# Kernel optimization log

Hardware: AMD Instinct MI355X
Metric: run time of the kernel (lower is better)

## Reference

```python
import jax, jax.numpy as jnp
import numpy as np

N = 100000      # nodes
E = 320000      # edges
D = 128         # num_node_in_embeddings
DE = 256        # num_edge_in_embeddings = 2*D
NOBJ = 160
NREL = 27
BN_EPS = 1e-5   # eval-mode BatchNorm with running_mean=0, running_var=1


def setup_inputs() -> dict:
    key = jax.random.key(0)
    ks = jax.random.split(key, 24)
    f32 = jnp.float32
    def rn(k, shape, scale=0.05):
        return jax.random.normal(k, shape, f32) * scale
    return {
        "node_feats": jax.random.normal(ks[0], (N, D), f32),
        "edge_index": jax.random.randint(ks[1], (E, 2), 0, N),
        # GCNConv layers (W: [in,out], bias)
        "gcn1_W": rn(ks[2], (D, D // 2)), "gcn1_b": rn(ks[3], (D // 2,)),
        "gcn2_W": rn(ks[4], (D // 2, D)), "gcn2_b": rn(ks[5], (D,)),
        # edge attention (Linear(DE, D//2))
        "eattn_W": rn(ks[6], (DE, D // 2)), "eattn_b": rn(ks[7], (D // 2,)),
        # node attention (Linear(D, DE//2)) and indicator reduction (Linear(DE, DE//2))
        "nattn_W": rn(ks[8], (D, DE // 2)), "nattn_b": rn(ks[9], (DE // 2,)),
        "nred_W": rn(ks[10], (DE, DE // 2)), "nred_b": rn(ks[11], (DE // 2,)),
        # edge MLPs (1x1 Conv1d == Linear)
        "emlp1_W": rn(ks[12], (DE, DE // 2)), "emlp1_b": rn(ks[13], (DE // 2,)),
        "emlp2_W": rn(ks[14], (DE // 2, DE)), "emlp2_b": rn(ks[15], (DE,)),
        # node classification head
        "nlin1_W": rn(ks[16], (D, D // 2)),
        "nbn_g": jnp.ones((D // 2,), f32) + rn(ks[17], (D // 2,)),
        "nbn_b": rn(ks[18], (D // 2,)),
        "nlin2_W": rn(ks[19], (D // 2, NOBJ)),
        # edge classification head
        "elin1_W": rn(ks[20], (DE, DE // 2)),
        "ebn_g": jnp.ones((DE // 2,), f32) + rn(ks[21], (DE // 2,)),
        "ebn_b": rn(ks[22], (DE // 2,)),
        "elin2_W": rn(ks[23], (DE // 2, NREL)),
    }


def _seg_mean(vals, idx, n):
    # torch_scatter 'mean': sum / clamp(count, 1)
    s = jax.ops.segment_sum(vals, idx, num_segments=n)
    c = jax.ops.segment_sum(jnp.ones((vals.shape[0], 1), vals.dtype), idx, num_segments=n)
    return s / jnp.maximum(c, 1.0)


def _gcn_conv(x, src, dst, W, b, n):
    # PyG GCNConv, add_self_loops=True, symmetric normalization.
    lin = x @ W
    deg = jax.ops.segment_sum(jnp.ones((src.shape[0],), x.dtype), dst, num_segments=n) + 1.0
    dis = jax.lax.rsqrt(deg)                       # deg^{-1/2}, includes self-loop
    norm = dis[src] * dis[dst]                     # per-edge norm
    agg = jax.ops.segment_sum(lin[src] * norm[:, None], dst, num_segments=n)
    return agg + lin * (dis * dis)[:, None] + b    # self-loop term + bias


def _bn_eval(x, g, b):
    # eval-mode BatchNorm1d with running_mean=0, running_var=1
    return x * (g / jnp.sqrt(1.0 + BN_EPS)) + b


def reference(node_feats, edge_index, gcn1_W, gcn1_b, gcn2_W, gcn2_b,
              eattn_W, eattn_b, nattn_W, nattn_b, nred_W, nred_b,
              emlp1_W, emlp1_b, emlp2_W, emlp2_b,
              nlin1_W, nbn_g, nbn_b, nlin2_W,
              elin1_W, ebn_g, ebn_b, elin2_W):
    n = node_feats.shape[0]
    src = edge_index[:, 0]
    dst = edge_index[:, 1]

    # edge feature init: [subject, object - subject]  -> [E, DE]
    subj = node_feats[src]
    edge_feats = jnp.concatenate([subj, node_feats[dst] - subj], axis=1)

    # edge attention -> scatter-mean indicators over rows/cols -> node gate
    edge_ind = edge_feats @ eattn_W + eattn_b            # [E, D/2]
    row = _seg_mean(edge_ind, src, n)                    # [N, D/2]
    col = _seg_mean(edge_ind, dst, n)                    # [N, D/2]
    agg_edge_indicator = jax.nn.sigmoid(row * col)

    # two GCN layers (dropout is identity in eval mode)
    h = jax.nn.relu(_gcn_conv(node_feats, src, dst, gcn1_W, gcn1_b, n)) * agg_edge_indicator
    h = jax.nn.relu(_gcn_conv(h, src, dst, gcn2_W, gcn2_b, n))           # [N, D]

    # node attention -> per-edge gate
    node_ind = jax.nn.relu(h @ nattn_W + nattn_b)                        # [N, DE/2]
    econcat = jnp.concatenate([node_ind[src], node_ind[dst]], axis=1)    # [E, DE]
    agg_node_indicator = jax.nn.sigmoid(econcat @ nred_W + nred_b)       # [E, DE/2]

    # edge MLPs (1x1 convs == linears over edges)
    ef = jax.nn.relu(edge_feats @ emlp1_W + emlp1_b) * agg_node_indicator
    ef = jax.nn.relu(ef @ emlp2_W + emlp2_b)                             # [E, DE]

    # node head: linear -> BN(eval) -> leaky_relu(0.2) -> linear -> softmax over classes
    nx = jax.nn.leaky_relu(_bn_eval(h @ nlin1_W, nbn_g, nbn_b), 0.2)
    node_logits = jax.nn.softmax(nx @ nlin2_W, axis=1)                   # [N, NOBJ]

    # edge head: note original applies softmax on dim=1 of [1,E,NREL] -> over EDGES
    ex = jax.nn.leaky_relu(_bn_eval(ef @ elin1_W, ebn_g, ebn_b), 0.2)
    edge_logits = jax.nn.softmax(ex @ elin2_W, axis=0)                   # [E, NREL]

    return (node_logits, edge_logits)
```

## Files before the change

kernel.cpp:

```cpp
#include <hip/hip_runtime.h>

#define NN 100000
#define EE 320000

typedef unsigned int uint32;
typedef __attribute__((ext_vector_type(8))) short bf16x8;
typedef __attribute__((ext_vector_type(4))) float f32x4;

__device__ __forceinline__ float4 ld4(const float* p){ return *(const float4*)p; }
__device__ __forceinline__ void st4(float* p, const float4 v){ *(float4*)p = v; }
__device__ __forceinline__ float sigm(float x){ return 1.f/(1.f + expf(-x)); }
__device__ __forceinline__ short f2b(float f){
  union { float f; uint32 u; } v; v.f = f;
  uint32 r = (v.u + 0x7FFFu + ((v.u>>16)&1u)) >> 16;
  return (short)r;
}

constexpr int EM_STORE=0, EM_BRELU=1, EM_BNLK=2;

template<int K,int NOUT,int EM>
__global__ __launch_bounds__(256) void gemm_k(
    const float* __restrict__ A,
    const float* __restrict__ W, const float* __restrict__ bias,
    const float* __restrict__ bng,
    float* __restrict__ C, int M)
{
  constexpr int CN = NOUT/16;
  __shared__ float As[16][68];
  __shared__ float Ws[16][NOUT];
  const int t  = threadIdx.x;
  const int tx = t & 15, ty = t >> 4;
  const int row0 = blockIdx.x * 64;

  float acc[4][CN];
  #pragma unroll
  for (int i=0;i<4;i++)
    #pragma unroll
    for (int j=0;j<CN;j++) acc[i][j]=0.f;

  const int r_st  = t >> 2;
  const int kq_st = (t & 3) * 4;

  for (int k0=0;k0<K;k0+=16) {
    {
      float4 v = make_float4(0.f,0.f,0.f,0.f);
      const int gr = row0 + r_st;
      if (gr < M) v = ld4(A + (size_t)gr*K + k0 + kq_st);
      As[kq_st+0][r_st]=v.x; As[kq_st+1][r_st]=v.y;
      As[kq_st+2][r_st]=v.z; As[kq_st+3][r_st]=v.w;
    }
    {
      constexpr int C4 = NOUT/4;
      for (int i=t;i<16*C4;i+=256){ int kk=i/C4, c4=(i%C4)*4;
        st4(&Ws[kk][c4], ld4(W + (size_t)(k0+kk)*NOUT + c4)); }
    }
    __syncthreads();
    #pragma unroll
    for (int kk=0;kk<16;kk++){
      float a0,a1,a2,a3;
      { const float4 av = *(const float4*)&As[kk][ty*4]; a0=av.x;a1=av.y;a2=av.z;a3=av.w; }
      float b[CN];
      if constexpr ((CN & 3) == 0) {
        #pragma unroll
        for (int j4=0;j4<CN;j4+=4){
          const float4 bv = *(const float4*)&Ws[kk][tx*CN+j4];
          b[j4]=bv.x;b[j4+1]=bv.y;b[j4+2]=bv.z;b[j4+3]=bv.w; }
      } else {
        #pragma unroll
        for (int j=0;j<CN;j++) b[j]=Ws[kk][tx*CN+j];
      }
      #pragma unroll
      for (int j=0;j<CN;j++){
        acc[0][j]=fmaf(a0,b[j],acc[0][j]);
        acc[1][j]=fmaf(a1,b[j],acc[1][j]);
        acc[2][j]=fmaf(a2,b[j],acc[2][j]);
        acc[3][j]=fmaf(a3,b[j],acc[3][j]);
      }
    }
    __syncthreads();
  }

  float sc[CN], sh[CN];
  if constexpr (EM==EM_BNLK) {
    const float r_ = rsqrtf(1.f + 1e-5f);
    #pragma unroll
    for (int j=0;j<CN;j++){ int c=tx*CN+j; sc[j]=bng[c]*r_; sh[j]=bias[c]; }
  }
  #pragma unroll
  for (int i=0;i<4;i++){
    const int r  = row0 + ty*4+i;
    if (r >= M) continue;
    #pragma unroll
    for (int j=0;j<CN;j++){
      const int c = tx*CN+j;
      float v = acc[i][j];
      if constexpr (EM==EM_BRELU) v = fmaxf(v + bias[c], 0.f);
      else if constexpr (EM==EM_BNLK){ float x = fmaf(v, sc[j], sh[j]); v = (x>0.f)? x : 0.2f*x; }
      C[(size_t)r*NOUT + c] = v;
    }
  }
}

__global__ void k_hist(const int* __restrict__ eidx, int* cntS, int* cntD, int E){
  int e = blockIdx.x*256+threadIdx.x; if (e>=E) return;
  atomicAdd(&cntS[eidx[2*e]], 1);
  atomicAdd(&cntD[eidx[2*e+1]], 1);
}
__global__ void k_scan_sum(const int* __restrict__ cnt, int* bsum, int n){
  __shared__ int red[256];
  const int b=blockIdx.x, t=threadIdx.x;
  int s=0;
  for (int i=b*1024+t; i<n && i<(b+1)*1024; i+=256) s += cnt[i];
  red[t]=s; __syncthreads();
  for (int o=128;o;o>>=1){ if(t<o) red[t]+=red[t+o]; __syncthreads(); }
  if (t==0) bsum[b]=red[0];
}
__global__ void k_scan_top(int* bsum, int nb){
  __shared__ int sh[256];
  const int t=threadIdx.x;
  int v=(t<nb)?bsum[t]:0;
  sh[t]=v; __syncthreads();
  for (int o=1;o<256;o<<=1){
    int u=0; if(t>=o) u=sh[t-o];
    __syncthreads();
    sh[t]+=u;
    __syncthreads();
  }
  if (t<nb) bsum[t]=sh[t]-v;
}
__global__ void k_scan_out(const int* __restrict__ cnt, const int* __restrict__ bofs,
                           int* __restrict__ off, int n){
  __shared__ int sh[256];
  const int b=blockIdx.x, t=threadIdx.x;
  const int base=b*1024+t*4;
  int c0=0,c1=0,c2=0,c3=0;
  if(base+0<n)c0=cnt[base+0];
  if(base+1<n)c1=cnt[base+1];
  if(base+2<n)c2=cnt[base+2];
  if(base+3<n)c3=cnt[base+3];
  int s=c0+c1+c2+c3;
  sh[t]=s; __syncthreads();
  int v=s;
  for (int o=1;o<256;o<<=1){
    int u=0; if(t>=o) u=sh[t-o];
    __syncthreads();
    sh[t]+=u;
    __syncthreads();
  }
  const int tofs = sh[t]-v + bofs[b];
  if(base+0<n) off[base+0]=tofs;
  if(base+1<n) off[base+1]=tofs+c0;
  if(base+2<n) off[base+2]=tofs+c0+c1;
  if(base+3<n) off[base+3]=tofs+c0+c1+c2;
}
__global__ void k_copyoff(const int* __restrict__ off, int* __restrict__ cur, int n, int E){
  int i=blockIdx.x*256+threadIdx.x;
  if (i<n) cur[i]=off[i];
}
__global__ void k_setend(int* offS, int* offD, int n, int E){
  if (threadIdx.x==0 && blockIdx.x==0){ offS[n]=E; offD[n]=E; }
}
__global__ void k_fill(const int* __restrict__ eidx, int* curS, int* curD,
                       int* __restrict__ csrS, int* __restrict__ csrD, int E){
  int e=blockIdx.x*256+threadIdx.x; if (e>=E) return;
  const int s=eidx[2*e], d=eidx[2*e+1];
  csrS[atomicAdd(&curS[s],1)] = d;
  csrD[atomicAdd(&curD[d],1)] = s;
}
__global__ void k_dis(const int* __restrict__ cntD, float* __restrict__ dis, int n){
  int i=blockIdx.x*256+threadIdx.x; if(i>=n)return;
  dis[i]=rsqrtf((float)cntD[i]+1.f);
}

__global__ void k_wprep(const float* __restrict__ eattnW, const float* __restrict__ gcn1W,
                        float* __restrict__ Wcat){
  int idx=blockIdx.x*256+threadIdx.x; if (idx>=128*192) return;
  int k=idx/192, c=idx-k*192;
  float v;
  if (c<64)       v = eattnW[(size_t)(128+k)*64 + c];
  else if (c<128) v = eattnW[(size_t)k*64 + (c-64)] - eattnW[(size_t)(128+k)*64 + (c-64)];
  else            v = gcn1W[(size_t)k*64 + (c-128)];
  Wcat[idx]=v;
}

template<int NC>
__global__ void k_gather(const float* __restrict__ src, int stride, int colbase,
                         const int* __restrict__ off, const int* __restrict__ csr,
                         float* __restrict__ out, int n){
  constexpr int TPN = NC/4;
  const int t=threadIdx.x;
  const int node = blockIdx.x*(256/TPN) + t/TPN; if (node>=n) return;
  const int cq = (t%TPN)*4;
  const int j1=off[node+1];
  float4 acc = make_float4(0.f,0.f,0.f,0.f);
  for (int j=off[node]; j<j1; ++j){
    const float4 v = ld4(src + (size_t)csr[j]*stride + colbase + cq);
    acc.x+=v.x; acc.y+=v.y; acc.z+=v.z; acc.w+=v.w;
  }
  st4(out + (size_t)node*NC + cq, acc);
}

__global__ void k_aei3(const float* __restrict__ TUL, const float* __restrict__ Q,
                       const float* __restrict__ S, const int* __restrict__ cntS,
                       const int* __restrict__ cntD, const float* __restrict__ bias,
                       float* __restrict__ aei, int n){
  int idx=blockIdx.x*256+threadIdx.x; if (idx>=n*16) return;
  const int i=idx>>4, cq=(idx&15)*4;
  const float cS=(float)cntS[i], cD=(float)cntD[i];
  const float iS=1.f/fmaxf(cS,1.f), iD=1.f/fmaxf(cD,1.f);
  const float* tul = TUL + (size_t)i*192;
  const float4 T4=ld4(tul+cq), U4=ld4(tul+64+cq);
  const float4 Q4=ld4(Q+(size_t)i*64+cq), S4=ld4(S+(size_t)i*64+cq), b4=ld4(bias+cq);
  float4 o;
  o.x=sigm(((cS*(U4.x+b4.x)+Q4.x)*iS) * ((cD*(T4.x+b4.x)+S4.x)*iD));
  o.y=sigm(((cS*(U4.y+b4.y)+Q4.y)*iS) * ((cD*(T4.y+b4.y)+S4.y)*iD));
  o.z=sigm(((cS*(U4.z+b4.z)+Q4.z)*iS) * ((cD*(T4.z+b4.z)+S4.z)*iD));
  o.w=sigm(((cS*(U4.w+b4.w)+Q4.w)*iS) * ((cD*(T4.w+b4.w)+S4.w)*iD));
  st4(aei + (size_t)i*64 + cq, o);
}

template<int NC, bool AEI>
__global__ void k_gcnagg(const float* __restrict__ lin, int stride, int colbase,
                         const int* __restrict__ off, const int* __restrict__ csr,
                         const float* __restrict__ dis, const float* __restrict__ aei,
                         const float* __restrict__ bias, float* __restrict__ h, int n){
  constexpr int TPN = NC/4;
  const int t=threadIdx.x;
  const int node = blockIdx.x*(256/TPN) + t/TPN; if (node>=n) return;
  const int cq = (t%TPN)*4;
  const int j1=off[node+1];
  float4 acc = make_float4(0.f,0.f,0.f,0.f);
  for (int j=off[node]; j<j1; ++j){
    const int s=csr[j];
    const float w=dis[s];
    const float4 v = ld4(lin + (size_t)s*stride + colbase + cq);
    acc.x=fmaf(v.x,w,acc.x); acc.y=fmaf(v.y,w,acc.y);
    acc.z=fmaf(v.z,w,acc.z); acc.w=fmaf(v.w,w,acc.w);
  }
  const float dn=dis[node], d2=dn*dn;
  const float4 own=ld4(lin + (size_t)node*stride + colbase + cq), b4=ld4(bias+cq);
  float4 o;
  o.x=fmaxf(fmaf(acc.x,dn,fmaf(own.x,d2,b4.x)),0.f);
  o.y=fmaxf(fmaf(acc.y,dn,fmaf(own.y,d2,b4.y)),0.f);
  o.z=fmaxf(fmaf(acc.z,dn,fmaf(own.z,d2,b4.z)),0.f);
  o.w=fmaxf(fmaf(acc.w,dn,fmaf(own.w,d2,b4.w)),0.f);
  if (AEI){ const float4 m=ld4(aei+(size_t)node*NC+cq); o.x*=m.x;o.y*=m.y;o.z*=m.z;o.w*=m.w; }
  st4(h + (size_t)node*NC + cq, o);
}

__global__ void k_twt(const float* __restrict__ W, short* __restrict__ Wt,
                      int K, int N, int NP){
  int idx = blockIdx.x*256 + threadIdx.x;
  if (idx >= NP*K) return;
  int n = idx / K, k = idx - n*K;
  Wt[idx] = (n<N)? f2b(W[(size_t)k*N + n]) : (short)0;
}

template<int KTOT, int NCT>
__device__ __forceinline__ void mm_phase(
    const short* __restrict__ Wt,
    short (*As)[264], short (*Bs)[128][40],
    int t, int lane, int arow, int kgrp, f32x4* acc)
{
  constexpr int KS = KTOT/32;
  constexpr int NC = NCT*16;
  const bool act = (t < NC*4);
  const int col = t>>2, q = t&3;
  const short* wp = Wt + (size_t)col*KTOT + q*8;
  float4 r;
  if (act){
    r = *(const float4*)wp;
    *(float4*)&Bs[0][col][q*8] = r;
  }
  __syncthreads();
  #pragma unroll
  for (int kb=0; kb<KS; ++kb){
    if (act && kb+1<KS) r = *(const float4*)(wp + (kb+1)*32);
    const bf16x8 a = *(const bf16x8*)&As[arow][kb*32 + kgrp*8];
    #pragma unroll
    for (int ct=0; ct<NCT; ++ct){
      const bf16x8 b = *(const bf16x8*)&Bs[kb&1][ct*16 + (lane&15)][kgrp*8];
      acc[ct] = __builtin_amdgcn_mfma_f32_16x16x32_bf16(a, b, acc[ct], 0, 0, 0);
    }
    if (act && kb+1<KS) *(float4*)&Bs[(kb+1)&1][col][q*8] = r;
    __syncthreads();
  }
}

__global__ __launch_bounds__(512) void k_edge(
  const float* __restrict__ nf, const float* __restrict__ ni,
  const int* __restrict__ eidx,
  const short* __restrict__ wt_nred, const float* __restrict__ nredb,
  const short* __restrict__ wt_e1,   const float* __restrict__ e1b,
  const short* __restrict__ wt_e2,   const float* __restrict__ e2b,
  const short* __restrict__ wt_l1,   const float* __restrict__ ebng, const float* __restrict__ ebnb,
  const short* __restrict__ wt_l2,
  float* __restrict__ elog)
{
  __shared__ short As[128][264];
  __shared__ short Bs[2][128][40];
  __shared__ int sidx[128], didx[128];
  const int t = threadIdx.x;
  const int lane = t & 63, wave = t >> 6;
  const int tile = wave >> 2, wv = wave & 3;
  const int row0 = blockIdx.x * 128;
  const int kgrp = lane >> 4;
  const int arow = tile*64 + wv*16 + (lane & 15);
  const int crow = tile*64 + wv*16 + kgrp*4;

  if (t < 128){ sidx[t]=eidx[2*(row0+t)]; didx[t]=eidx[2*(row0+t)+1]; }
  __syncthreads();

  const int srow = t >> 2, seg = t & 3;

  {
    const float* src = (seg<2)? (ni + (size_t)sidx[srow]*128 + seg*64)
                              : (ni + (size_t)didx[srow]*128 + (seg-2)*64);
    short* dst = &As[srow][seg*64];
    #pragma unroll
    for (int p=0;p<8;p++){
      float4 u = ld4(src + p*8), v = ld4(src + p*8 + 4);
      bf16x8 o;
      o[0]=f2b(u.x);o[1]=f2b(u.y);o[2]=f2b(u.z);o[3]=f2b(u.w);
      o[4]=f2b(v.x);o[5]=f2b(v.y);o[6]=f2b(v.z);o[7]=f2b(v.w);
      *(bf16x8*)(dst + p*8) = o;
    }
  }
  f32x4 acc1[8];
  #pragma unroll
  for (int j=0;j<8;j++) acc1[j] = (f32x4){0.f,0.f,0.f,0.f};
  mm_phase<256,8>(wt_nred, As, Bs, t, lane, arow, kgrp, acc1);

  float g[8][4];
  #pragma unroll
  for (int ct=0;ct<8;ct++){
    const float bb = nredb[ct*16 + (lane&15)];
    #pragma unroll
    for (int r=0;r<4;r++) g[ct][r] = sigm(acc1[ct][r] + bb);
  }

  {
    short* dst = &As[srow][seg*64];
    const int s = sidx[srow], d = didx[srow];
    #pragma unroll
    for (int p=0;p<8;p++){
      float4 u, v;
      if (seg < 2){
        u = ld4(nf + (size_t)s*128 + seg*64 + p*8);
        v = ld4(nf + (size_t)s*128 + seg*64 + p*8 + 4);
      } else {
        float4 ua = ld4(nf + (size_t)d*128 + (seg-2)*64 + p*8);
        float4 ub = ld4(nf + (size_t)s*128 + (seg-2)*64 + p*8);
        float4 va = ld4(nf + (size_t)d*128 + (seg-2)*64 + p*8 + 4);
        float4 vb = ld4(nf + (size_t)s*128 + (seg-2)*64 + p*8 + 4);
        u.x=ua.x-ub.x; u.y=ua.y-ub.y; u.z=ua.z-ub.z; u.w=ua.w-ub.w;
        v.x=va.x-vb.x; v.y=va.y-vb.y; v.z=va.z-vb.z; v.w=va.w-vb.w;
      }
      bf16x8 o;
      o[0]=f2b(u.x);o[1]=f2b(u.y);o[2]=f2b(u.z);o[3]=f2b(u.w);
      o[4]=f2b(v.x);o[5]=f2b(v.y);o[6]=f2b(v.z);o[7]=f2b(v.w);
      *(bf16x8*)(dst + p*8) = o;
    }
  }
  f32x4 acc2[8];
  #pragma unroll
  for (int j=0;j<8;j++) acc2[j] = (f32x4){0.f,0.f,0.f,0.f};
  mm_phase<256,8>(wt_e1, As, Bs, t, lane, arow, kgrp, acc2);

  #pragma unroll
  for (int ct=0;ct<8;ct++){
    const int col = ct*16 + (lane&15);
    const float bb = e1b[col];
    #pragma unroll
    for (int r=0;r<4;r++)
      As[crow+r][col] = f2b(fmaxf(acc2[ct][r] + bb, 0.f) * g[ct][r]);
  }

  f32x4 acc3[16];
  #pragma unroll
  for (int j=0;j<16;j++) acc3[j] = (f32x4){0.f,0.f,0.f,0.f};
  mm_phase<128,8>(wt_e2,                    As, Bs, t, lane, arow, kgrp, acc3);
  mm_phase<128,8>(wt_e2 + (size_t)128*128,  As, Bs, t, lane, arow, kgrp, acc3+8);
  #pragma unroll
  for (int ct=0;ct<16;ct++){
    const int col = ct*16 + (lane&15);
    const float bb = e2b[col];
    #pragma unroll
    for (int r=0;r<4;r++)
      As[crow+r][col] = f2b(fmaxf(acc3[ct][r] + bb, 0.f));
  }

  f32x4 acc4[8];
  #pragma unroll
  for (int j=0;j<8;j++) acc4[j] = (f32x4){0.f,0.f,0.f,0.f};
  mm_phase<256,8>(wt_l1, As, Bs, t, lane, arow, kgrp, acc4);
  {
    const float r_ = rsqrtf(1.f + 1e-5f);
    #pragma unroll
    for (int ct=0;ct<8;ct++){
      const int col = ct*16 + (lane&15);
      const float sc = ebng[col]*r_, sh = ebnb[col];
      #pragma unroll
      for (int r=0;r<4;r++){
        float x = fmaf(acc4[ct][r], sc, sh);
        As[crow+r][col] = f2b((x>0.f)? x : 0.2f*x);
      }
    }
  }

  f32x4 acc5[2];
  acc5[0] = (f32x4){0.f,0.f,0.f,0.f}; acc5[1] = (f32x4){0.f,0.f,0.f,0.f};
  mm_phase<128,2>(wt_l2, As, Bs, t, lane, arow, kgrp, acc5);

  float* Lb = (float*)&As[0][0];
  #pragma unroll
  for (int ct=0;ct<2;ct++){
    const int col = ct*16 + (lane&15);
    if (col < 27){
      #pragma unroll
      for (int r=0;r<4;r++) Lb[(crow+r)*28 + col] = acc5[ct][r];
    }
  }
  __syncthreads();
  for (int i=t; i<128*27; i+=512){
    int rr = i/27, cc = i - rr*27;
    elog[(size_t)(row0+rr)*27 + cc] = Lb[rr*28 + cc];
  }
}

__global__ __launch_bounds__(256) void k_softmax_row(float* __restrict__ x, int M){
  const int wave = threadIdx.x>>6, lane = threadIdx.x&63;
  const int r = blockIdx.x*4 + wave; if (r>=M) return;
  float* p = x + (size_t)r*160;
  float v0 = p[lane], v1 = p[64+lane];
  float v2 = (lane<32)? p[128+lane] : -3.4e38f;
  float m = fmaxf(fmaxf(v0,v1),v2);
  for (int o=32;o;o>>=1) m = fmaxf(m, __shfl_xor(m,o));
  float e0=expf(v0-m), e1=expf(v1-m), e2=(lane<32)?expf(v2-m):0.f;
  float s=e0+e1+e2;
  for (int o=32;o;o>>=1) s += __shfl_xor(s,o);
  float inv = 1.f/s;
  p[lane]=e0*inv; p[64+lane]=e1*inv; if(lane<32)p[128+lane]=e2*inv;
}
__global__ void k_colmax(const float* __restrict__ x, uint32* __restrict__ cmax_u, int E){
  __shared__ float red[8][32];
  const int t=threadIdx.x, col=t&31, seg=t>>5;
  float m = -3.4e38f;
  if (col < 27)
    for (int r = blockIdx.x*8 + seg; r < E; r += gridDim.x*8)
      m = fmaxf(m, x[(size_t)r*27+col]);
  red[seg][col]=m; __syncthreads();
  if (t<32){
    float mm=red[0][t];
    #pragma unroll
    for (int s2=1;s2<8;s2++) mm=fmaxf(mm,red[s2][t]);
    if (t<27){
      uint32 u=__float_as_uint(mm);
      u = (u&0x80000000u)? ~u : (u|0x80000000u);
      atomicMax(&cmax_u[t], u);
    }
  }
}
__global__ void k_colfix(const uint32* __restrict__ cmax_u, float* __restrict__ cmaxf){
  int t=threadIdx.x; if (t>=27) return;
  uint32 u=cmax_u[t];
  cmaxf[t] = (u&0x80000000u)? __uint_as_float(u&0x7FFFFFFFu) : __uint_as_float(~u);
}
__global__ void k_colsum(const float* __restrict__ x, const float* __restrict__ cmaxf,
                         float* __restrict__ csum, int E){
  __shared__ float red[8][32];
  const int t=threadIdx.x, col=t&31, seg=t>>5;
  float s = 0.f;
  if (col < 27){
    const float cm = cmaxf[col];
    for (int r = blockIdx.x*8 + seg; r < E; r += gridDim.x*8)
      s += expf(x[(size_t)r*27+col] - cm);
  }
  red[seg][col]=s; __syncthreads();
  if (t<32){
    float ss=red[0][t];
    #pragma unroll
    for (int s2=1;s2<8;s2++) ss+=red[s2][t];
    if (t<27) atomicAdd(&csum[t], ss);
  }
}
__global__ void k_colnorm(float* __restrict__ x, const float* __restrict__ cmaxf,
                          const float* __restrict__ csum, int E){
  int idx=blockIdx.x*256+threadIdx.x;
  if (idx >= E*27) return;
  int c = idx - (idx/27)*27;
  x[idx] = expf(x[idx]-cmaxf[c]) / csum[c];
}

extern "C" void kernel_launch(void* const* d_in, const int* in_sizes, int n_in,
                              void* d_out, int out_size, void* d_ws, size_t ws_size,
                              hipStream_t stream)
{
  const float* nf     = (const float*)d_in[0];
  const int*   eidx   = (const int*)  d_in[1];
  const float* gcn1W  = (const float*)d_in[2];
  const float* gcn1b  = (const float*)d_in[3];
  const float* gcn2W  = (const float*)d_in[4];
  const float* gcn2b  = (const float*)d_in[5];
  const float* eattnW = (const float*)d_in[6];
  const float* eattnb = (const float*)d_in[7];
  const float* nattnW = (const float*)d_in[8];
  const float* nattnb = (const float*)d_in[9];
  const float* nredW  = (const float*)d_in[10];
  const float* nredb  = (const float*)d_in[11];
  const float* emlp1W = (const float*)d_in[12];
  const float* emlp1b = (const float*)d_in[13];
  const float* emlp2W = (const float*)d_in[14];
  const float* emlp2b = (const float*)d_in[15];
  const float* nlin1W = (const float*)d_in[16];
  const float* nbng   = (const float*)d_in[17];
  const float* nbnb   = (const float*)d_in[18];
  const float* nlin2W = (const float*)d_in[19];
  const float* elin1W = (const float*)d_in[20];
  const float* ebng   = (const float*)d_in[21];
  const float* ebnb   = (const float*)d_in[22];
  const float* elin2W = (const float*)d_in[23];
  (void)in_sizes; (void)n_in; (void)out_size; (void)ws_size;

  const int N = NN, E = EE;
  float* out  = (float*)d_out;
  float* nlog = out;
  float* elog = out + (size_t)N*160;

  float* ws   = (float*)d_ws;
  float* h2   = ws;
  float* lin2 = ws + (size_t)N*128;
  float* Q    = lin2;
  float* S    = lin2 + (size_t)N*64;
  float* niB  = lin2;
  float* nx   = lin2;
  float* TUL  = ws + (size_t)N*256;
  float* h1   = ws + (size_t)N*448;
  float* aei  = ws + (size_t)N*512;
  float* dis  = ws + (size_t)N*576;
  float* smalls = ws + (size_t)N*577;
  float* Wcat = smalls + 128;
  int*   ip   = (int*)(Wcat + 24576);
  int* cntS = ip;
  int* cntD = ip + N;
  int* offS = ip + 2*N;
  int* offD = ip + 3*N + 64;
  int* curS = ip + 4*N + 128;
  int* curD = ip + 5*N + 128;
  int* csrS = ip + 6*N + 128;
  int* csrD = ip + 6*N + 128 + E;
  int* bsum = ip + 6*N + 128 + 2*E;
  short* wtb  = (short*)(bsum + 256);
  short* wt_nred = wtb;
  short* wt_e1   = wtb + 32768;
  short* wt_e2   = wtb + 65536;
  short* wt_l1   = wtb + 98304;
  short* wt_l2   = wtb + 131072;

  const int NB1024 = (N + 1023)/1024;

  k_twt<<<128,256,0,stream>>>(nredW,  wt_nred, 256, 128, 128);
  k_twt<<<128,256,0,stream>>>(emlp1W, wt_e1,   256, 128, 128);
  k_twt<<<128,256,0,stream>>>(emlp2W, wt_e2,   128, 256, 256);
  k_twt<<<128,256,0,stream>>>(elin1W, wt_l1,   256, 128, 128);
  k_twt<<<16, 256,0,stream>>>(elin2W, wt_l2,   128, 27,  32);
  k_wprep<<<96,256,0,stream>>>(eattnW, gcn1W, Wcat);

  (void)hipMemsetAsync(cntS, 0, 2*(size_t)N*sizeof(int), stream);
  k_hist<<<(E+255)/256,256,0,stream>>>(eidx, cntS, cntD, E);
  k_scan_sum<<<NB1024,256,0,stream>>>(cntS, bsum, N);
  k_scan_top<<<1,256,0,stream>>>(bsum, NB1024);
  k_scan_out<<<NB1024,256,0,stream>>>(cntS, bsum, offS, N);
  k_scan_sum<<<NB1024,256,0,stream>>>(cntD, bsum, N);
  k_scan_top<<<1,256,0,stream>>>(bsum, NB1024);
  k_scan_out<<<NB1024,256,0,stream>>>(cntD, bsum, offD, N);
  k_setend<<<1,64,0,stream>>>(offS, offD, N, E);
  k_copyoff<<<(N+255)/256,256,0,stream>>>(offS, curS, N, E);
  k_copyoff<<<(N+255)/256,256,0,stream>>>(offD, curD, N, E);
  k_fill<<<(E+255)/256,256,0,stream>>>(eidx, curS, curD, csrS, csrD, E);
  k_dis<<<(N+255)/256,256,0,stream>>>(cntD, dis, N);

  gemm_k<128,192,EM_STORE><<<(N+63)/64,256,0,stream>>>(nf, Wcat, nullptr, nullptr, TUL, N);

  k_gather<64><<<(N+15)/16,256,0,stream>>>(TUL, 192, 0,  offS, csrS, Q, N);
  k_gather<64><<<(N+15)/16,256,0,stream>>>(TUL, 192, 64, offD, csrD, S, N);
  k_aei3<<<(N*16+255)/256,256,0,stream>>>(TUL, Q, S, cntS, cntD, eattnb, aei, N);

  k_gcnagg<64,true><<<(N+15)/16,256,0,stream>>>(TUL, 192, 128, offD, csrD, dis, aei, gcn1b, h1, N);

  gemm_k<64,128,EM_STORE><<<(N+63)/64,256,0,stream>>>(h1, gcn2W, nullptr, nullptr, lin2, N);
  k_gcnagg<128,false><<<(N+7)/8,256,0,stream>>>(lin2, 128, 0, offD, csrD, dis, nullptr, gcn2b, h2, N);

  gemm_k<128,128,EM_BRELU><<<(N+63)/64,256,0,stream>>>(h2, nattnW, nattnb, nullptr, niB, N);

  k_edge<<<E/128,512,0,stream>>>(
      nf, niB, eidx,
      wt_nred, nredb, wt_e1, emlp1b, wt_e2, emlp2b,
      wt_l1, ebng, ebnb, wt_l2, elog);

  gemm_k<128,64,EM_BNLK><<<(N+63)/64,256,0,stream>>>(h2, nlin1W, nbnb, nbng, nx, N);
  gemm_k<64,160,EM_STORE><<<(N+63)/64,256,0,stream>>>(nx, nlin2W, nullptr, nullptr, nlog, N);
  k_softmax_row<<<(N+3)/4,256,0,stream>>>(nlog, N);

  (void)hipMemsetAsync(smalls, 0, 96*sizeof(float), stream);
  k_colmax<<<1024,256,0,stream>>>(elog, (uint32*)smalls, E);
  k_colfix<<<1,32,0,stream>>>((const uint32*)smalls, smalls+64);
  k_colsum<<<1024,256,0,stream>>>(elog, smalls+64, smalls+32, E);
  k_colnorm<<<(E*27+255)/256,256,0,stream>>>(elog, smalls+64, smalls+32, E);
}
```

Before: 911.4 us.

## Switch fused edge kernel to 32x32x16 MFMA with 256-thread blocks

Rewrites the fused edge MLP kernel to use 32x32x16 bf16 MFMA tiles with four waves per 128-edge block instead of 16x16x32 tiles with eight waves. The sigmoid gate is packed into bf16 pairs to cut register use. The emlp2 output halves are written into swapped column ranges of the shared tile, and the elin1 weight rows are rotated by 128 to compensate. Larger MFMA tiles reduce LDS operand reads per FLOP and the smaller block may raise occupancy, but each thread does more staging work and carries larger accumulators.

```diff
diff --git a/kernel.cpp b/kernel.cpp
--- a/kernel.cpp
+++ b/kernel.cpp
@@ -6,6 +6,7 @@
 typedef unsigned int uint32;
 typedef __attribute__((ext_vector_type(8))) short bf16x8;
 typedef __attribute__((ext_vector_type(4))) float f32x4;
+typedef __attribute__((ext_vector_type(16))) float f32x16;
 
 __device__ __forceinline__ float4 ld4(const float* p){ return *(const float4*)p; }
 __device__ __forceinline__ void st4(float* p, const float4 v){ *(float4*)p = v; }
@@ -153,7 +154,7 @@
   if(base+2<n) off[base+2]=tofs+c0+c1;
   if(base+3<n) off[base+3]=tofs+c0+c1+c2;
 }
-__global__ void k_copyoff(const int* __restrict__ off, int* __restrict__ cur, int n, int E){
+__global__ void k_copyoff(const int* __restrict__ off, int* __restrict__ cur, int n){
   int i=blockIdx.x*256+threadIdx.x;
   if (i<n) cur[i]=off[i];
 }
@@ -249,45 +250,52 @@
 }
 
 __global__ void k_twt(const float* __restrict__ W, short* __restrict__ Wt,
-                      int K, int N, int NP){
+                      int K, int N, int NP, int krot){
   int idx = blockIdx.x*256 + threadIdx.x;
   if (idx >= NP*K) return;
   int n = idx / K, k = idx - n*K;
-  Wt[idx] = (n<N)? f2b(W[(size_t)k*N + n]) : (short)0;
-}
-
-template<int KTOT, int NCT>
-__device__ __forceinline__ void mm_phase(
+  int ks = k + krot; if (ks >= K) ks -= K;
+  Wt[idx] = (n<N)? f2b(W[(size_t)ks*N + n]) : (short)0;
+}
+
+template<int KTOT, int NT>
+__device__ __forceinline__ void mm32(
     const short* __restrict__ Wt,
-    short (*As)[264], short (*Bs)[128][40],
-    int t, int lane, int arow, int kgrp, f32x4* acc)
+    short (*As)[264], short (*Bs)[128][24],
+    int t, int lane, int w, f32x16* acc)
 {
-  constexpr int KS = KTOT/32;
-  constexpr int NC = NCT*16;
-  const bool act = (t < NC*4);
-  const int col = t>>2, q = t&3;
-  const short* wp = Wt + (size_t)col*KTOT + q*8;
+  constexpr int STEPS = KTOT/16;
+  constexpr int NC = NT*32;
+  const int lane31 = lane & 31, kh = lane >> 5;
+  const int arow = w*32 + lane31;
+  const bool act = (t < NC*2);
+  const int col = t >> 1, half = t & 1;
+  const short* wp = Wt + (size_t)col*KTOT + half*8;
   float4 r;
   if (act){
     r = *(const float4*)wp;
-    *(float4*)&Bs[0][col][q*8] = r;
+    *(float4*)&Bs[0][col][half*8] = r;
   }
   __syncthreads();
   #pragma unroll
-  for (int kb=0; kb<KS; ++kb){
-    if (act && kb+1<KS) r = *(const float4*)(wp + (kb+1)*32);
-    const bf16x8 a = *(const bf16x8*)&As[arow][kb*32 + kgrp*8];
-    #pragma unroll
-    for (int ct=0; ct<NCT; ++ct){
-      const bf16x8 b = *(const bf16x8*)&Bs[kb&1][ct*16 + (lane&15)][kgrp*8];
-      acc[ct] = __builtin_amdgcn_mfma_f32_16x16x32_bf16(a, b, acc[ct], 0, 0, 0);
-    }
-    if (act && kb+1<KS) *(float4*)&Bs[(kb+1)&1][col][q*8] = r;
+  for (int ks=0; ks<STEPS; ++ks){
+    if (act && ks+1<STEPS) r = *(const float4*)(wp + (ks+1)*16);
+    const bf16x8 a = *(const bf16x8*)&As[arow][ks*16 + kh*8];
+    #pragma unroll
+    for (int ct=0; ct<NT; ++ct){
+      const bf16x8 b = *(const bf16x8*)&Bs[ks&1][ct*32 + lane31][kh*8];
+      acc[ct] = __builtin_amdgcn_mfma_f32_32x32x16_bf16(a, b, acc[ct], 0, 0, 0);
+    }
+    if (act && ks+1<STEPS) *(float4*)&Bs[(ks+1)&1][col][half*8] = r;
     __syncthreads();
   }
 }
 
-__global__ __launch_bounds__(512) void k_edge(
+__device__ __forceinline__ int rowof(int reg, int kh){
+  return (reg & 3) + ((reg >> 2) << 3) + (kh << 2);
+}
+
+__global__ __launch_bounds__(256) void k_edge(
   const float* __restrict__ nf, const float* __restrict__ ni,
   const int* __restrict__ eidx,
   const short* __restrict__ wt_nred, const float* __restrict__ nredb,
@@ -298,27 +306,20 @@
   float* __restrict__ elog)
 {
   __shared__ short As[128][264];
-  __shared__ short Bs[2][128][40];
-  __shared__ int sidx[128], didx[128];
+  __shared__ short Bs[2][128][24];
   const int t = threadIdx.x;
-  const int lane = t & 63, wave = t >> 6;
-  const int tile = wave >> 2, wv = wave & 3;
+  const int lane = t & 63, w = t >> 6;
   const int row0 = blockIdx.x * 128;
-  const int kgrp = lane >> 4;
-  const int arow = tile*64 + wv*16 + (lane & 15);
-  const int crow = tile*64 + wv*16 + kgrp*4;
-
-  if (t < 128){ sidx[t]=eidx[2*(row0+t)]; didx[t]=eidx[2*(row0+t)+1]; }
-  __syncthreads();
-
-  const int srow = t >> 2, seg = t & 3;
+  const int lane31 = lane & 31, kh = lane >> 5;
+
+  const int srow = t >> 1, sseg = t & 1;
+  const int s_s = eidx[2*(row0+srow)], s_d = eidx[2*(row0+srow)+1];
 
   {
-    const float* src = (seg<2)? (ni + (size_t)sidx[srow]*128 + seg*64)
-                              : (ni + (size_t)didx[srow]*128 + (seg-2)*64);
-    short* dst = &As[srow][seg*64];
-    #pragma unroll
-    for (int p=0;p<8;p++){
+    const float* src = sseg ? (ni + (size_t)s_d*128) : (ni + (size_t)s_s*128);
+    short* dst = &As[srow][sseg*128];
+    #pragma unroll
+    for (int p=0;p<16;p++){
       float4 u = ld4(src + p*8), v = ld4(src + p*8 + 4);
       bf16x8 o;
       o[0]=f2b(u.x);o[1]=f2b(u.y);o[2]=f2b(u.z);o[3]=f2b(u.w);
@@ -326,33 +327,36 @@
       *(bf16x8*)(dst + p*8) = o;
     }
   }
-  f32x4 acc1[8];
-  #pragma unroll
-  for (int j=0;j<8;j++) acc1[j] = (f32x4){0.f,0.f,0.f,0.f};
-  mm_phase<256,8>(wt_nred, As, Bs, t, lane, arow, kgrp, acc1);
-
-  float g[8][4];
-  #pragma unroll
-  for (int ct=0;ct<8;ct++){
-    const float bb = nredb[ct*16 + (lane&15)];
-    #pragma unroll
-    for (int r=0;r<4;r++) g[ct][r] = sigm(acc1[ct][r] + bb);
+  f32x16 acc[4];
+  #pragma unroll
+  for (int j=0;j<4;j++) acc[j] = (f32x16)(0.f);
+  mm32<256,4>(wt_nred, As, Bs, t, lane, w, acc);
+
+  uint32 gp[4][8];
+  #pragma unroll
+  for (int ct=0;ct<4;ct++){
+    const float bb = nredb[ct*32 + lane31];
+    #pragma unroll
+    for (int rq=0;rq<8;rq++){
+      const uint32 g0 = (uint32)(unsigned short)f2b(sigm(acc[ct][2*rq]   + bb));
+      const uint32 g1 = (uint32)(unsigned short)f2b(sigm(acc[ct][2*rq+1] + bb));
+      gp[ct][rq] = g0 | (g1<<16);
+    }
   }
 
   {
-    short* dst = &As[srow][seg*64];
-    const int s = sidx[srow], d = didx[srow];
-    #pragma unroll
-    for (int p=0;p<8;p++){
+    short* dst = &As[srow][sseg*128];
+    #pragma unroll
+    for (int p=0;p<16;p++){
       float4 u, v;
-      if (seg < 2){
-        u = ld4(nf + (size_t)s*128 + seg*64 + p*8);
-        v = ld4(nf + (size_t)s*128 + seg*64 + p*8 + 4);
+      if (sseg == 0){
+        u = ld4(nf + (size_t)s_s*128 + p*8);
+        v = ld4(nf + (size_t)s_s*128 + p*8 + 4);
       } else {
-        float4 ua = ld4(nf + (size_t)d*128 + (seg-2)*64 + p*8);
-        float4 ub = ld4(nf + (size_t)s*128 + (seg-2)*64 + p*8);
-        float4 va = ld4(nf + (size_t)d*128 + (seg-2)*64 + p*8 + 4);
-        float4 vb = ld4(nf + (size_t)s*128 + (seg-2)*64 + p*8 + 4);
+        float4 ua = ld4(nf + (size_t)s_d*128 + p*8);
+        float4 ub = ld4(nf + (size_t)s_s*128 + p*8);
+        float4 va = ld4(nf + (size_t)s_d*128 + p*8 + 4);
+        float4 vb = ld4(nf + (size_t)s_s*128 + p*8 + 4);
         u.x=ua.x-ub.x; u.y=ua.y-ub.y; u.z=ua.z-ub.z; u.w=ua.w-ub.w;
         v.x=va.x-vb.x; v.y=va.y-vb.y; v.z=va.z-vb.z; v.w=va.w-vb.w;
       }
@@ -362,67 +366,73 @@
       *(bf16x8*)(dst + p*8) = o;
     }
   }
-  f32x4 acc2[8];
-  #pragma unroll
-  for (int j=0;j<8;j++) acc2[j] = (f32x4){0.f,0.f,0.f,0.f};
-  mm_phase<256,8>(wt_e1, As, Bs, t, lane, arow, kgrp, acc2);
-
-  #pragma unroll
-  for (int ct=0;ct<8;ct++){
-    const int col = ct*16 + (lane&15);
+  #pragma unroll
+  for (int j=0;j<4;j++) acc[j] = (f32x16)(0.f);
+  mm32<256,4>(wt_e1, As, Bs, t, lane, w, acc);
+
+  #pragma unroll
+  for (int ct=0;ct<4;ct++){
+    const int col = ct*32 + lane31;
     const float bb = e1b[col];
     #pragma unroll
-    for (int r=0;r<4;r++)
-      As[crow+r][col] = f2b(fmaxf(acc2[ct][r] + bb, 0.f) * g[ct][r]);
-  }
-
-  f32x4 acc3[16];
-  #pragma unroll
-  for (int j=0;j<16;j++) acc3[j] = (f32x4){0.f,0.f,0.f,0.f};
-  mm_phase<128,8>(wt_e2,                    As, Bs, t, lane, arow, kgrp, acc3);
-  mm_phase<128,8>(wt_e2 + (size_t)128*128,  As, Bs, t, lane, arow, kgrp, acc3+8);
-  #pragma unroll
-  for (int ct=0;ct<16;ct++){
-    const int col = ct*16 + (lane&15);
+    for (int reg=0;reg<16;reg++){
+      const uint32 u = gp[ct][reg>>1];
+      const float gv = __uint_as_float((reg&1) ? (u & 0xFFFF0000u) : (u<<16));
+      As[w*32 + rowof(reg,kh)][col] = f2b(fmaxf(acc[ct][reg] + bb, 0.f) * gv);
+    }
+  }
+
+  #pragma unroll
+  for (int j=0;j<4;j++) acc[j] = (f32x16)(0.f);
+  mm32<128,4>(wt_e2, As, Bs, t, lane, w, acc);
+  #pragma unroll
+  for (int ct=0;ct<4;ct++){
+    const int col = ct*32 + lane31;
     const float bb = e2b[col];
     #pragma unroll
-    for (int r=0;r<4;r++)
-      As[crow+r][col] = f2b(fmaxf(acc3[ct][r] + bb, 0.f));
-  }
-
-  f32x4 acc4[8];
-  #pragma unroll
-  for (int j=0;j<8;j++) acc4[j] = (f32x4){0.f,0.f,0.f,0.f};
-  mm_phase<256,8>(wt_l1, As, Bs, t, lane, arow, kgrp, acc4);
+    for (int reg=0;reg<16;reg++)
+      As[w*32 + rowof(reg,kh)][128+col] = f2b(fmaxf(acc[ct][reg] + bb, 0.f));
+  }
+  #pragma unroll
+  for (int j=0;j<4;j++) acc[j] = (f32x16)(0.f);
+  mm32<128,4>(wt_e2 + (size_t)128*128, As, Bs, t, lane, w, acc);
+  #pragma unroll
+  for (int ct=0;ct<4;ct++){
+    const int col = ct*32 + lane31;
+    const float bb = e2b[128+col];
+    #pragma unroll
+    for (int reg=0;reg<16;reg++)
+      As[w*32 + rowof(reg,kh)][col] = f2b(fmaxf(acc[ct][reg] + bb, 0.f));
+  }
+
+  #pragma unroll
+  for (int j=0;j<4;j++) acc[j] = (f32x16)(0.f);
+  mm32<256,4>(wt_l1, As, Bs, t, lane, w, acc);
   {
     const float r_ = rsqrtf(1.f + 1e-5f);
     #pragma unroll
-    for (int ct=0;ct<8;ct++){
-      const int col = ct*16 + (lane&15);
+    for (int ct=0;ct<4;ct++){
+      const int col = ct*32 + lane31;
       const float sc = ebng[col]*r_, sh = ebnb[col];
       #pragma unroll
-      for (int r=0;r<4;r++){
-        float x = fmaf(acc4[ct][r], sc, sh);
-        As[crow+r][col] = f2b((x>0.f)? x : 0.2f*x);
+      for (int reg=0;reg<16;reg++){
+        float x = fmaf(acc[ct][reg], sc, sh);
+        As[w*32 + rowof(reg,kh)][col] = f2b((x>0.f)? x : 0.2f*x);
       }
     }
   }
 
-  f32x4 acc5[2];
-  acc5[0] = (f32x4){0.f,0.f,0.f,0.f}; acc5[1] = (f32x4){0.f,0.f,0.f,0.f};
-  mm_phase<128,2>(wt_l2, As, Bs, t, lane, arow, kgrp, acc5);
+  f32x16 acc5 = (f32x16)(0.f);
+  mm32<128,1>(wt_l2, As, Bs, t, lane, w, &acc5);
 
   float* Lb = (float*)&As[0][0];
-  #pragma unroll
-  for (int ct=0;ct<2;ct++){
-    const int col = ct*16 + (lane&15);
-    if (col < 27){
-      #pragma unroll
-      for (int r=0;r<4;r++) Lb[(crow+r)*28 + col] = acc5[ct][r];
-    }
+  if (lane31 < 27){
+    #pragma unroll
+    for (int reg=0;reg<16;reg++)
+      Lb[(w*32 + rowof(reg,kh))*28 + lane31] = acc5[reg];
   }
   __syncthreads();
-  for (int i=t; i<128*27; i+=512){
+  for (int i=t; i<128*27; i+=256){
     int rr = i/27, cc = i - rr*27;
     elog[(size_t)(row0+rr)*27 + cc] = Lb[rr*28 + cc];
   }
@@ -559,11 +569,11 @@
 
   const int NB1024 = (N + 1023)/1024;
 
-  k_twt<<<128,256,0,stream>>>(nredW,  wt_nred, 256, 128, 128);
-  k_twt<<<128,256,0,stream>>>(emlp1W, wt_e1,   256, 128, 128);
-  k_twt<<<128,256,0,stream>>>(emlp2W, wt_e2,   128, 256, 256);
-  k_twt<<<128,256,0,stream>>>(elin1W, wt_l1,   256, 128, 128);
-  k_twt<<<16, 256,0,stream>>>(elin2W, wt_l2,   128, 27,  32);
+  k_twt<<<128,256,0,stream>>>(nredW,  wt_nred, 256, 128, 128, 0);
+  k_twt<<<128,256,0,stream>>>(emlp1W, wt_e1,   256, 128, 128, 0);
+  k_twt<<<128,256,0,stream>>>(emlp2W, wt_e2,   128, 256, 256, 0);
+  k_twt<<<128,256,0,stream>>>(elin1W, wt_l1,   256, 128, 128, 128);
+  k_twt<<<16, 256,0,stream>>>(elin2W, wt_l2,   128, 27,  32,  0);
   k_wprep<<<96,256,0,stream>>>(eattnW, gcn1W, Wcat);
 
   (void)hipMemsetAsync(cntS, 0, 2*(size_t)N*sizeof(int), stream);
@@ -575,8 +585,8 @@
   k_scan_top<<<1,256,0,stream>>>(bsum, NB1024);
   k_scan_out<<<NB1024,256,0,stream>>>(cntD, bsum, offD, N);
   k_setend<<<1,64,0,stream>>>(offS, offD, N, E);
-  k_copyoff<<<(N+255)/256,256,0,stream>>>(offS, curS, N, E);
-  k_copyoff<<<(N+255)/256,256,0,stream>>>(offD, curD, N, E);
+  k_copyoff<<<(N+255)/256,256,0,stream>>>(offS, curS, N);
+  k_copyoff<<<(N+255)/256,256,0,stream>>>(offD, curD, N);
   k_fill<<<(E+255)/256,256,0,stream>>>(eidx, curS, curD, csrS, csrD, E);
   k_dis<<<(N+255)/256,256,0,stream>>>(cntD, dis, N);
 
@@ -593,7 +603,7 @@
 
   gemm_k<128,128,EM_BRELU><<<(N+63)/64,256,0,stream>>>(h2, nattnW, nattnb, nullptr, niB, N);
 
-  k_edge<<<E/128,512,0,stream>>>(
+  k_edge<<<E/128,256,0,stream>>>(
       nf, niB, eidx,
       wt_nred, nredb, wt_e1, emlp1b, wt_e2, emlp2b,
       wt_l1, ebng, ebnb, wt_l2, elog);
```

Result: slower. 975.4 us (+7.0%).
